# Kernel optimization log

Hardware: AMD Instinct MI355X
Metric: run time of the kernel (lower is better)

## Reference

```python
import jax, jax.numpy as jnp
import numpy as np
import math

L = 16.0
DT = 1.0
TAU = 10.0
THRESHOLD = 1.0
ALPHA = 0.01
DECAY = math.exp(-DT / TAU)

@jax.custom_vjp
def multibit_spike(x):
    # forward: floor(x) clipped to [0, L]
    return jnp.clip(jnp.floor(x), 0.0, L)

def _spike_fwd(x):
    return multibit_spike(x), x

def _spike_bwd(x, g):
    dist = jnp.abs(x - jnp.round(x))
    scale = jnp.clip(1.0 - 2.0 * dist, 0.0, 1.0)
    in_range = ((x >= 0.0) & (x <= L + 1.0)).astype(g.dtype)
    return (g * in_range * scale,)

multibit_spike.defvjp(_spike_fwd, _spike_bwd)

def setup_inputs() -> dict:
    key = jax.random.key(0)
    k_x, k_w = jax.random.split(key)
    B, T, IN, H = 16, 2048, 512, 512
    # SNN-aware init: std = 0.5*threshold / (sqrt(fan_in)*0.3)
    std = 0.5 * THRESHOLD / (math.sqrt(IN) * 0.3)
    x = jax.random.normal(k_x, (B, T, IN), dtype=jnp.float32)
    W = jax.random.normal(k_w, (H, IN), dtype=jnp.float32) * std
    b = jnp.zeros((H,), dtype=jnp.float32)
    return {"x": x, "W": W, "b": b}

def reference(x, W, b):
    B, T, _ = x.shape
    Hd = W.shape[0]
    # batched linear projection of the whole sequence (compute-heavy GEMM)
    h = jnp.einsum('bti,hi->bth', x, W) + b  # [B, T, H]
    v0 = jnp.zeros((B, Hd), dtype=x.dtype)
    theta0 = jnp.full((B, Hd), THRESHOLD, dtype=x.dtype)

    def step(carry, i_t):
        v, theta = carry
        v = v * DECAY + i_t
        clamp_limit = L * theta * 2.0
        v = jnp.clip(v, -clamp_limit, clamp_limit)
        spike = multibit_spike(v / theta)
        v = v - spike * theta
        theta = theta + ALPHA * spike - ALPHA * (theta - THRESHOLD)
        return (v, theta), spike

    (v_f, theta_f), spikes_tbh = jax.lax.scan(step, (v0, theta0), jnp.swapaxes(h, 0, 1))
    spikes = jnp.swapaxes(spikes_tbh, 0, 1)  # [B, T, H]
    return spikes, v_f, theta_f
```

## Files before the change

### kernel.cpp

```cpp
#include <hip/hip_runtime.h>

#define B_  16
#define T_  2048
#define IN_ 512
#define H_  512
#define M_  (B_ * T_)

#define BM 128
#define BN 128
#define BK 16
#define LDT (BM + 4)

static __device__ __forceinline__ float4 ld4(const float* p) {
    return *reinterpret_cast<const float4*>(p);
}

__global__ __launch_bounds__(256)
void gemm_xwT(const float* __restrict__ X, const float* __restrict__ W,
              const float* __restrict__ bias, float* __restrict__ Hout) {
    __shared__ float As[BK][LDT];
    __shared__ float Bs[BK][LDT];

    const int tid = threadIdx.x;

    const int L  = blockIdx.y * gridDim.x + blockIdx.x;
    const int r  = L & 7;
    const int q  = L >> 3;
    const int mt = r + 8 * (q >> 2);
    const int nt = q & 3;
    const int m0 = mt * BM;
    const int n0 = nt * BN;

    const int tx = tid & 15;
    const int ty = tid >> 4;

    const int row = tid >> 2;
    const int kph = (tid & 3) * 4;

    const float* pa0 = X + (size_t)(m0 + row) * IN_ + kph;
    const float* pa1 = pa0 + (size_t)64 * IN_;
    const float* pb0 = W + (size_t)(n0 + row) * IN_ + kph;
    const float* pb1 = pb0 + (size_t)64 * IN_;

    float4 ra0 = ld4(pa0), ra1 = ld4(pa1), rb0 = ld4(pb0), rb1 = ld4(pb1);

    float acc[8][8];
#pragma unroll
    for (int i = 0; i < 8; ++i)
#pragma unroll
        for (int j = 0; j < 8; ++j) acc[i][j] = 0.0f;

    for (int k0 = 0; k0 < IN_; k0 += BK) {
        As[kph + 0][row]      = ra0.x;  As[kph + 1][row]      = ra0.y;
        As[kph + 2][row]      = ra0.z;  As[kph + 3][row]      = ra0.w;
        As[kph + 0][row + 64] = ra1.x;  As[kph + 1][row + 64] = ra1.y;
        As[kph + 2][row + 64] = ra1.z;  As[kph + 3][row + 64] = ra1.w;
        Bs[kph + 0][row]      = rb0.x;  Bs[kph + 1][row]      = rb0.y;
        Bs[kph + 2][row]      = rb0.z;  Bs[kph + 3][row]      = rb0.w;
        Bs[kph + 0][row + 64] = rb1.x;  Bs[kph + 1][row + 64] = rb1.y;
        Bs[kph + 2][row + 64] = rb1.z;  Bs[kph + 3][row + 64] = rb1.w;
        __syncthreads();

        if (k0 + BK < IN_) {
            ra0 = ld4(pa0 + k0 + BK);  ra1 = ld4(pa1 + k0 + BK);
            rb0 = ld4(pb0 + k0 + BK);  rb1 = ld4(pb1 + k0 + BK);
        }

#pragma unroll
        for (int k = 0; k < BK; ++k) {
            float4 av0 = ld4(&As[k][ty * 4]);
            float4 av1 = ld4(&As[k][ty * 4 + 64]);
            float4 bv0 = ld4(&Bs[k][tx * 4]);
            float4 bv1 = ld4(&Bs[k][tx * 4 + 64]);
            const float am[8] = {av0.x, av0.y, av0.z, av0.w,
                                 av1.x, av1.y, av1.z, av1.w};
            const float bn8[8] = {bv0.x, bv0.y, bv0.z, bv0.w,
                                  bv1.x, bv1.y, bv1.z, bv1.w};
#pragma unroll
            for (int i = 0; i < 8; ++i)
#pragma unroll
                for (int j = 0; j < 8; ++j)
                    acc[i][j] = fmaf(am[i], bn8[j], acc[i][j]);
        }
        __syncthreads();
    }

    float4 bb0 = ld4(&bias[n0 + tx * 4]);
    float4 bb1 = ld4(&bias[n0 + tx * 4 + 64]);
#pragma unroll
    for (int i = 0; i < 8; ++i) {
        const int r2 = m0 + ((i < 4) ? (ty * 4 + i) : (64 + ty * 4 + (i - 4)));
        float4 o0, o1;
        o0.x = acc[i][0] + bb0.x;  o0.y = acc[i][1] + bb0.y;
        o0.z = acc[i][2] + bb0.z;  o0.w = acc[i][3] + bb0.w;
        o1.x = acc[i][4] + bb1.x;  o1.y = acc[i][5] + bb1.y;
        o1.z = acc[i][6] + bb1.z;  o1.w = acc[i][7] + bb1.w;
        *reinterpret_cast<float4*>(&Hout[(size_t)r2 * H_ + n0 + tx * 4])      = o0;
        *reinterpret_cast<float4*>(&Hout[(size_t)r2 * H_ + n0 + tx * 4 + 64]) = o1;
    }
}

#define SPF 32

__device__ __forceinline__
void scan_compute(const float* __restrict__ buf, float* __restrict__ sarr,
                  float& v, float& theta) {
    const float DECAY_F = 0.9048374180359595f;
    const float ALPHA_F = 0.01f;
#pragma unroll
    for (int j = 0; j < SPF; ++j) {
        float cur = buf[j];
        v = v * DECAY_F + cur;
        float cl = 32.0f * theta;
        v = __builtin_amdgcn_fmed3f(v, -cl, cl);

        float r0 = __builtin_amdgcn_rcpf(theta);
        float q0 = v * r0;
        float er = fmaf(-theta, q0, v);
        float q  = fmaf(er, r0, q0);

        float s = floorf(q);
        s = __builtin_amdgcn_fmed3f(s, 0.0f, 16.0f);
        v = v - s * theta;
        theta = theta + ALPHA_F * s - ALPHA_F * (theta - 1.0f);
        sarr[j] = s;
    }
}

__device__ __forceinline__
void store_batch(float* __restrict__ sp, int tb, const float* __restrict__ sarr) {
#pragma unroll
    for (int j = 0; j < SPF; ++j)
        sp[(size_t)(tb + j) * H_] = sarr[j];
}

__global__ __launch_bounds__(64, 1)
void gif_scan(const float* __restrict__ Hbuf, float* __restrict__ spikes,
              float* __restrict__ vout, float* __restrict__ thout) {
    const int gid = blockIdx.x * 64 + threadIdx.x;
    const int b = gid >> 9;
    const int h = gid & 511;

    const float* ip = Hbuf   + (size_t)b * T_ * H_ + h;
    float*       sp = spikes + (size_t)b * T_ * H_ + h;

    float bufA[SPF], bufB[SPF], sA[SPF], sB[SPF];
#pragma unroll
    for (int j = 0; j < SPF; ++j) bufA[j] = ip[(size_t)j * H_];

    float v = 0.0f, theta = 1.0f;
    for (int t0 = 0; t0 < T_; t0 += 2 * SPF) {
#pragma unroll
        for (int j = 0; j < SPF; ++j) bufB[j] = ip[(size_t)(t0 + SPF + j) * H_];
        asm volatile("" ::: "memory");

        scan_compute(bufA, sA, v, theta);
        store_batch(sp, t0, sA);

        if (t0 + 2 * SPF < T_) {
#pragma unroll
            for (int j = 0; j < SPF; ++j)
                bufA[j] = ip[(size_t)(t0 + 2 * SPF + j) * H_];
        }
        asm volatile("" ::: "memory");

        scan_compute(bufB, sB, v, theta);
        store_batch(sp, t0 + SPF, sB);
    }
    vout[gid]  = v;
    thout[gid] = theta;
}

extern "C" void kernel_launch(void* const* d_in, const int* in_sizes, int n_in,
                              void* d_out, int out_size, void* d_ws, size_t ws_size,
                              hipStream_t stream) {
    const float* x    = (const float*)d_in[0];
    const float* W    = (const float*)d_in[1];
    const float* bias = (const float*)d_in[2];

    float* out    = (float*)d_out;
    float* spikes = out;
    float* v_f    = out + (size_t)M_ * H_;
    float* th_f   = v_f + (size_t)B_ * H_;

    float* hbuf   = (float*)d_ws;

    dim3 grid(M_ / BM, H_ / BN);
    gemm_xwT<<<grid, 256, 0, stream>>>(x, W, bias, hbuf);
    gif_scan<<<(B_ * H_) / 64, 64, 0, stream>>>(hbuf, spikes, v_f, th_f);
}
```

Baseline: 369.6 us.

## Fuse GEMM and scan into one persistent kernel with flag-based tile handoff

Merges the projection GEMM and the recurrent scan into a single launch. GEMM blocks produce tiles in time-chunk order and publish per-tile release flags, while 32 scan blocks spin on those flags and consume each 128-step chunk as soon as it is ready. The aim is to hide the latency-bound scan behind GEMM work instead of running the two phases back to back. It relies on scan blocks being co-resident with the GEMM blocks to avoid deadlock, and it uses 256-thread scan blocks in place of 64-thread ones, which changes how the scan is spread across CUs.

```diff
diff --git a/kernel.cpp b/kernel.cpp
--- a/kernel.cpp
+++ b/kernel.cpp
@@ -11,26 +11,21 @@
 #define BK 16
 #define LDT (BM + 4)
 
+#define NGEMM 512
+#define NSCAN 32
+
+__device__ unsigned g_flagA[1024];
+__device__ unsigned g_flagB[1024];
+
 static __device__ __forceinline__ float4 ld4(const float* p) {
     return *reinterpret_cast<const float4*>(p);
 }
 
-__global__ __launch_bounds__(256)
-void gemm_xwT(const float* __restrict__ X, const float* __restrict__ W,
-              const float* __restrict__ bias, float* __restrict__ Hout) {
-    __shared__ float As[BK][LDT];
-    __shared__ float Bs[BK][LDT];
-
-    const int tid = threadIdx.x;
-
-    const int L  = blockIdx.y * gridDim.x + blockIdx.x;
-    const int r  = L & 7;
-    const int q  = L >> 3;
-    const int mt = r + 8 * (q >> 2);
-    const int nt = q & 3;
-    const int m0 = mt * BM;
-    const int n0 = nt * BN;
-
+__device__ __forceinline__
+void gemm_tile(const float* __restrict__ X, const float* __restrict__ W,
+               const float* __restrict__ bias, float* __restrict__ Hout,
+               int m0, int n0, int tid,
+               float (*As)[LDT], float (*Bs)[LDT]) {
     const int tx = tid & 15;
     const int ty = tid >> 4;
 
@@ -100,15 +95,13 @@
     }
 }
 
-#define SPF 32
-
 __device__ __forceinline__
-void scan_compute(const float* __restrict__ buf, float* __restrict__ sarr,
-                  float& v, float& theta) {
+void scan_compute16(const float* __restrict__ buf, float* __restrict__ sarr,
+                    float& v, float& theta) {
     const float DECAY_F = 0.9048374180359595f;
     const float ALPHA_F = 0.01f;
 #pragma unroll
-    for (int j = 0; j < SPF; ++j) {
+    for (int j = 0; j < 16; ++j) {
         float cur = buf[j];
         v = v * DECAY_F + cur;
         float cl = 32.0f * theta;
@@ -127,48 +120,85 @@
     }
 }
 
-__device__ __forceinline__
-void store_batch(float* __restrict__ sp, int tb, const float* __restrict__ sarr) {
-#pragma unroll
-    for (int j = 0; j < SPF; ++j)
-        sp[(size_t)(tb + j) * H_] = sarr[j];
-}
-
-__global__ __launch_bounds__(64, 1)
-void gif_scan(const float* __restrict__ Hbuf, float* __restrict__ spikes,
-              float* __restrict__ vout, float* __restrict__ thout) {
-    const int gid = blockIdx.x * 64 + threadIdx.x;
-    const int b = gid >> 9;
-    const int h = gid & 511;
-
-    const float* ip = Hbuf   + (size_t)b * T_ * H_ + h;
-    float*       sp = spikes + (size_t)b * T_ * H_ + h;
-
-    float bufA[SPF], bufB[SPF], sA[SPF], sB[SPF];
-#pragma unroll
-    for (int j = 0; j < SPF; ++j) bufA[j] = ip[(size_t)j * H_];
-
-    float v = 0.0f, theta = 1.0f;
-    for (int t0 = 0; t0 < T_; t0 += 2 * SPF) {
-#pragma unroll
-        for (int j = 0; j < SPF; ++j) bufB[j] = ip[(size_t)(t0 + SPF + j) * H_];
-        asm volatile("" ::: "memory");
-
-        scan_compute(bufA, sA, v, theta);
-        store_batch(sp, t0, sA);
-
-        if (t0 + 2 * SPF < T_) {
-#pragma unroll
-            for (int j = 0; j < SPF; ++j)
-                bufA[j] = ip[(size_t)(t0 + 2 * SPF + j) * H_];
-        }
-        asm volatile("" ::: "memory");
-
-        scan_compute(bufB, sB, v, theta);
-        store_batch(sp, t0 + SPF, sB);
-    }
-    vout[gid]  = v;
-    thout[gid] = theta;
+__global__ __launch_bounds__(256, 3)
+void fused_gemm_scan(const float* __restrict__ X, const float* __restrict__ W,
+                     const float* __restrict__ bias, float* __restrict__ Hbuf,
+                     float* __restrict__ spikes, float* __restrict__ vout,
+                     float* __restrict__ thout) {
+    __shared__ float As[BK][LDT];
+    __shared__ float Bs[BK][LDT];
+
+    if (blockIdx.x < NGEMM) {
+        const int tid = threadIdx.x;
+        const int g   = blockIdx.x;
+        const int tt7 = g >> 6;
+        const int bb  = (g >> 2) & 15;
+        const int nt  = g & 3;
+#pragma unroll
+        for (int ph = 0; ph < 2; ++ph) {
+            const int tt = tt7 + ph * 8;
+            const int mt = bb * 16 + tt;
+            gemm_tile(X, W, bias, Hbuf, mt * BM, nt * BN, tid, As, Bs);
+            __syncthreads();
+            if (tid == 0) {
+                const int tau = mt * 4 + nt;
+                __hip_atomic_store(&g_flagA[tau], 1u, __ATOMIC_RELEASE,
+                                   __HIP_MEMORY_SCOPE_AGENT);
+                __hip_atomic_store(&g_flagB[tau], 1u, __ATOMIC_RELEASE,
+                                   __HIP_MEMORY_SCOPE_AGENT);
+            }
+        }
+    } else {
+        const int s   = blockIdx.x - NGEMM;
+        const int gid = s * 256 + (int)threadIdx.x;
+        const int b   = gid >> 9;
+        const int h   = gid & 511;
+
+        const float* ip = Hbuf   + (size_t)b * T_ * H_ + h;
+        float*       sp = spikes + (size_t)b * T_ * H_ + h;
+
+        unsigned* flagbase = ((h >> 6) & 1) ? g_flagB : g_flagA;
+        const int ntq = h >> 7;
+
+        float bufA[16], bufB[16], sA[16], sB[16];
+        float v = 0.0f, theta = 1.0f;
+
+        for (int c = 0; c < 16; ++c) {
+            const int t0 = c * 128;
+            unsigned* fp = flagbase + ((size_t)(b * 16 + c) * 4 + ntq);
+            while (__hip_atomic_load(fp, __ATOMIC_ACQUIRE,
+                                     __HIP_MEMORY_SCOPE_AGENT) == 0u)
+                __builtin_amdgcn_s_sleep(8);
+            __hip_atomic_store(fp, 0u, __ATOMIC_RELAXED,
+                               __HIP_MEMORY_SCOPE_AGENT);
+
+#pragma unroll
+            for (int j = 0; j < 16; ++j) bufA[j] = ip[(size_t)(t0 + j) * H_];
+            for (int bt = 0; bt < 8; bt += 2) {
+#pragma unroll
+                for (int j = 0; j < 16; ++j)
+                    bufB[j] = ip[(size_t)(t0 + (bt + 1) * 16 + j) * H_];
+                asm volatile("" ::: "memory");
+                scan_compute16(bufA, sA, v, theta);
+#pragma unroll
+                for (int j = 0; j < 16; ++j)
+                    sp[(size_t)(t0 + bt * 16 + j) * H_] = sA[j];
+
+                if (bt + 2 < 8) {
+#pragma unroll
+                    for (int j = 0; j < 16; ++j)
+                        bufA[j] = ip[(size_t)(t0 + (bt + 2) * 16 + j) * H_];
+                }
+                asm volatile("" ::: "memory");
+                scan_compute16(bufB, sB, v, theta);
+#pragma unroll
+                for (int j = 0; j < 16; ++j)
+                    sp[(size_t)(t0 + (bt + 1) * 16 + j) * H_] = sB[j];
+            }
+        }
+        vout[gid]  = v;
+        thout[gid] = theta;
+    }
 }
 
 extern "C" void kernel_launch(void* const* d_in, const int* in_sizes, int n_in,
@@ -185,7 +215,6 @@
 
     float* hbuf   = (float*)d_ws;
 
-    dim3 grid(M_ / BM, H_ / BN);
-    gemm_xwT<<<grid, 256, 0, stream>>>(x, W, bias, hbuf);
-    gif_scan<<<(B_ * H_) / 64, 64, 0, stream>>>(hbuf, spikes, v_f, th_f);
-}
+    fused_gemm_scan<<<NGEMM + NSCAN, 256, 0, stream>>>(
+        x, W, bias, hbuf, spikes, v_f, th_f);
+}
```

After: 812.2 us. 2.2x slower.
